# Optimization experiments

Hardware: AMD Instinct MI355X
Metric: run time of the kernel (lower is better)

Reference implementation:

```python
import jax, jax.numpy as jnp
import numpy as np

B = 2048   # number of samples; acts as seq_len for the (S,N,E) transformer
DIN = 768
D = 512    # hidden_dim
H = 8      # nheads
HD = D // H
L = 3      # encoder layers
P = 40     # num_prototypes
Q = D // 4 # 128, projected feature dim
EPS = 1e-5


def setup_inputs() -> dict:
    key = jax.random.key(0)
    ks = jax.random.split(key, 22)
    s = 0.02
    rn = lambda k, shape: jax.random.normal(k, shape, jnp.float32) * s
    return {
        "x": jax.random.normal(ks[0], (B, DIN), jnp.float32),
        "reduce_w": rn(ks[1], (D, DIN)), "reduce_b": rn(ks[2], (D,)),
        "in_w": rn(ks[3], (L, 3 * D, D)), "in_b": rn(ks[4], (L, 3 * D)),
        "out_w": rn(ks[5], (L, D, D)), "out_b": rn(ks[6], (L, D)),
        "ff1_w": rn(ks[7], (L, D, D)), "ff1_b": rn(ks[8], (L, D)),
        "ff2_w": rn(ks[9], (L, D, D)), "ff2_b": rn(ks[10], (L, D)),
        "ln1_w": jnp.ones((L, D), jnp.float32), "ln1_b": jnp.zeros((L, D), jnp.float32),
        "ln2_w": jnp.ones((L, D), jnp.float32), "ln2_b": jnp.zeros((L, D), jnp.float32),
        "mlp_w1": rn(ks[11], (D, D)), "mlp_b1": rn(ks[12], (D,)),
        "mlp_w2": rn(ks[13], (D, D)), "mlp_b2": rn(ks[14], (D,)),
        "mlp_w3": rn(ks[15], (Q, D)), "mlp_b3": rn(ks[16], (Q,)),
        "highlights": jax.random.normal(ks[17], (P, Q), jnp.float32),
        "negatives": jax.random.normal(ks[18], (P, Q), jnp.float32),
    }


def _inorm(x):
    # InstanceNorm1d (affine=False) on a 2D tensor: per-row normalize over last dim
    m = x.mean(-1, keepdims=True)
    v = ((x - m) ** 2).mean(-1, keepdims=True)  # biased variance, matches torch
    return (x - m) * jax.lax.rsqrt(v + EPS)


def _ln(x, w, b):
    m = x.mean(-1, keepdims=True)
    v = ((x - m) ** 2).mean(-1, keepdims=True)
    return (x - m) * jax.lax.rsqrt(v + EPS) * w + b


def _cdist(a, cb):
    # euclidean distances [B,P]
    d2 = (a * a).sum(-1, keepdims=True) + (cb * cb).sum(-1) - 2.0 * a @ cb.T
    return jnp.sqrt(jnp.maximum(d2, 0.0))


def reference(x, reduce_w, reduce_b, in_w, in_b, out_w, out_b,
              ff1_w, ff1_b, ff2_w, ff2_b, ln1_w, ln1_b, ln2_w, ln2_b,
              mlp_w1, mlp_b1, mlp_w2, mlp_b2, mlp_w3, mlp_b3,
              highlights, negatives):
    feat0 = _inorm(x @ reduce_w.T + reduce_b)  # [B,D]

    # TransformerEncoder, post-norm, relu FFN, dropout off (eval).
    # Input is (seq=B, batch=1, D) -> attention across all B rows.
    feat = feat0
    scale = 1.0 / np.sqrt(HD)
    for i in range(L):
        qkv = feat @ in_w[i].T + in_b[i]           # [B,3D]
        q, k, v = jnp.split(qkv, 3, axis=-1)
        q = q.reshape(B, H, HD)
        k = k.reshape(B, H, HD)
        v = v.reshape(B, H, HD)
        scores = jnp.einsum('ihd,jhd->hij', q, k) * scale  # [H,B,B]
        attn = jax.nn.softmax(scores, axis=-1)
        ctx = jnp.einsum('hij,jhd->ihd', attn, v).reshape(B, D)
        attn_out = ctx @ out_w[i].T + out_b[i]
        feat = _ln(feat + attn_out, ln1_w[i], ln1_b[i])
        ff = jax.nn.relu(feat @ ff1_w[i].T + ff1_b[i]) @ ff2_w[i].T + ff2_b[i]
        feat = _ln(feat + ff, ln2_w[i], ln2_b[i])

    feat = feat0 + _inorm(feat)

    # MLP 512 -> 512 -> 512 -> 128 (relu on all but last)
    feat = jax.nn.relu(feat @ mlp_w1.T + mlp_b1)
    feat = jax.nn.relu(feat @ mlp_w2.T + mlp_b2)
    feat = feat @ mlp_w3.T + mlp_b3
    feat = _inorm(feat)  # [B,Q]

    positive_dist = _cdist(feat, highlights).min(-1)
    negative_dist = _cdist(feat, negatives).min(-1)
    logits = jnp.stack([-negative_dist, -positive_dist], axis=-1)  # [B,2]
    return logits
```

## Files before the change

### kernel.cpp

```cpp
#include <hip/hip_runtime.h>
#include <math.h>
#include <cstddef>

#define EPS 1e-5f

typedef __attribute__((ext_vector_type(8))) short bf16x8;
typedef __attribute__((ext_vector_type(4))) float f32x4;

__device__ __forceinline__ float wave_sum(float v) {
#pragma unroll
  for (int o = 32; o > 0; o >>= 1) v += __shfl_xor(v, o, 64);
  return v;
}

__device__ __forceinline__ unsigned short f2b(float f) {
  union { float f; unsigned int u; } v; v.f = f;
  unsigned int r = (v.u + 0x7FFFu + ((v.u >> 16) & 1u)) >> 16;
  return (unsigned short)r;
}
__device__ __forceinline__ float b2f(unsigned short u) {
  union { unsigned int u; float f; } v; v.u = ((unsigned int)u) << 16;
  return v.f;
}

struct WConvArgs {
  const float* src[8];
  unsigned short* dst[8];
  int n[8];
};
__global__ __launch_bounds__(256) void conv_w(WConvArgs a) {
  const int arr = blockIdx.y;
  const int i = (blockIdx.x * 256 + threadIdx.x) * 4;
  if (i >= a.n[arr]) return;
  const float4 f = *(const float4*)(a.src[arr] + i);
  unsigned short t[4] = {f2b(f.x), f2b(f.y), f2b(f.z), f2b(f.w)};
  unsigned short* d = a.dst[arr] + i;
  *(ushort2*)d = *(ushort2*)&t[0];
  *(ushort2*)(d + 2) = *(ushort2*)&t[2];
}

template <int RELU, int AF32, int OUT_F32, int OUT_BF16, int MERGE, int RESID,
          int SCALEQ>
__global__ __launch_bounds__(256) void gemm32(
    const void* __restrict__ Aptr, const float* __restrict__ pmp,
    const unsigned short* __restrict__ W, const float* __restrict__ bias,
    const float* __restrict__ Rf, float* __restrict__ Cf,
    unsigned short* __restrict__ Cb, int M, int N, int K) {
  __shared__ __align__(16) unsigned short As[2][32][72];
  __shared__ __align__(16) unsigned short Ws[2][64][72];
  const int tid = threadIdx.x;
  const int wid = tid >> 6, lane = tid & 63;
  const int ln = lane & 15, quad = lane >> 4;
  const int m0 = blockIdx.x * 32, n0 = blockIdx.y * 64;
  const int arow = tid >> 3, aseg = tid & 7;
  const int wrow = tid >> 2, wseg = tid & 3;
  const int KS = K >> 6;

  bf16x8 ra;
  float4 ra32[2];
  bf16x8 rwb0, rwb1;
  bf16x8 rp[4];
  float rl;

  auto load_tile = [&](int ks) {
    const int k0 = ks * 64;
    if (MERGE) {
      const int h = ks;
      const int row = m0 + arow;
      rl = 0.f;
#pragma unroll
      for (int s = 0; s < 4; ++s) {
        const size_t b = (size_t)((s * 8 + h) * 2048 + row);
        rl += pmp[b];
        rp[s] = *(const bf16x8*)((const unsigned short*)Aptr + b * 64 + aseg * 8);
      }
    } else if (AF32) {
      const float* ap = (const float*)Aptr + (size_t)(m0 + arow) * K + k0 + aseg * 8;
      ra32[0] = *(const float4*)ap;
      ra32[1] = *(const float4*)(ap + 4);
    } else {
      ra = *(const bf16x8*)((const unsigned short*)Aptr +
                            (size_t)(m0 + arow) * K + k0 + aseg * 8);
    }
    const unsigned short* wp = W + (size_t)(n0 + wrow) * K + k0 + wseg * 16;
    rwb0 = *(const bf16x8*)wp;
    rwb1 = *(const bf16x8*)(wp + 8);
  };

  auto store_tile = [&](int buf) {
    if (MERGE) {
      float inv = 1.f / rl;
      unsigned short ta[8];
#pragma unroll
      for (int j = 0; j < 8; ++j) {
        float s = b2f((unsigned short)rp[0][j]) + b2f((unsigned short)rp[1][j]) +
                  b2f((unsigned short)rp[2][j]) + b2f((unsigned short)rp[3][j]);
        ta[j] = f2b(inv * s);
      }
      *(bf16x8*)&As[buf][arow][aseg * 8] = *(const bf16x8*)&ta[0];
    } else if (AF32) {
      unsigned short ta[8];
      ta[0] = f2b(ra32[0].x); ta[1] = f2b(ra32[0].y);
      ta[2] = f2b(ra32[0].z); ta[3] = f2b(ra32[0].w);
      ta[4] = f2b(ra32[1].x); ta[5] = f2b(ra32[1].y);
      ta[6] = f2b(ra32[1].z); ta[7] = f2b(ra32[1].w);
      *(bf16x8*)&As[buf][arow][aseg * 8] = *(const bf16x8*)&ta[0];
    } else {
      *(bf16x8*)&As[buf][arow][aseg * 8] = ra;
    }
    *(bf16x8*)&Ws[buf][wrow][wseg * 16] = rwb0;
    *(bf16x8*)&Ws[buf][wrow][wseg * 16 + 8] = rwb1;
  };

  f32x4 acc[2];
  acc[0] = (f32x4){0.f, 0.f, 0.f, 0.f};
  acc[1] = (f32x4){0.f, 0.f, 0.f, 0.f};

  const int mrow = (wid & 1) * 16, nh = wid >> 1;

  load_tile(0);
  store_tile(0);
  __syncthreads();

#pragma unroll 1
  for (int ks = 0; ks < KS; ++ks) {
    const int cur = ks & 1;
    if (ks + 1 < KS) load_tile(ks + 1);
#pragma unroll
    for (int kc = 0; kc < 2; ++kc) {
      bf16x8 af = *(const bf16x8*)&As[cur][mrow + ln][kc * 32 + quad * 8];
#pragma unroll
      for (int nt = 0; nt < 2; ++nt) {
        bf16x8 wf = *(const bf16x8*)&Ws[cur][nh * 32 + nt * 16 + ln][kc * 32 + quad * 8];
        acc[nt] = __builtin_amdgcn_mfma_f32_16x16x32_bf16(af, wf, acc[nt], 0, 0, 0);
      }
    }
    if (ks + 1 < KS) store_tile(cur ^ 1);
    __syncthreads();
  }

  const int gm = m0 + mrow + quad * 4;
  const float qs = (SCALEQ && n0 < 512) ? 0.125f : 1.f;
#pragma unroll
  for (int nt = 0; nt < 2; ++nt) {
    const int gn = n0 + nh * 32 + nt * 16 + ln;
    float bv = bias[gn];
#pragma unroll
    for (int r = 0; r < 4; ++r) {
      float v = acc[nt][r] + bv;
      if (SCALEQ) v *= qs;
      if (RELU) v = fmaxf(v, 0.f);
      if (RESID) v += Rf[(size_t)(gm + r) * N + gn];
      if (OUT_F32) Cf[(size_t)(gm + r) * N + gn] = v;
      if (OUT_BF16) Cb[(size_t)(gm + r) * N + gn] = f2b(v);
    }
  }
}

__global__ __launch_bounds__(256) void flash_attn7(
    const unsigned short* __restrict__ qkv, float* __restrict__ pm,
    unsigned short* __restrict__ po) {
  __shared__ __align__(16) unsigned short Ks[64][72];
  __shared__ __align__(16) unsigned short Vt[64][72];
  __shared__ __align__(16) unsigned short Ps[64][72];
  const int qt = blockIdx.x, h = blockIdx.y, sp = blockIdx.z;
  const int tid = threadIdx.x;
  const int wid = tid >> 6, lane = tid & 63;
  const int ln = lane & 15, quad = lane >> 4;
  const int wq0 = wid * 16;

  bf16x8 aq[2];
  {
    const unsigned short* qp =
        qkv + (size_t)(qt * 64 + wq0 + ln) * 1536 + h * 64 + quad * 8;
    aq[0] = *(const bf16x8*)qp;
    aq[1] = *(const bf16x8*)(qp + 32);
  }

  const int key = tid >> 2, seg = tid & 3;
  bf16x8 rk0, rk1;
  unsigned short tv[16];

  auto load_kv = [&](int t) {
    const int g = sp * 8 + t;
    const unsigned short* kr =
        qkv + (size_t)(g * 64 + key) * 1536 + 512 + h * 64 + seg * 16;
    rk0 = *(const bf16x8*)kr;
    rk1 = *(const bf16x8*)(kr + 8);
#pragma unroll
    for (int j = 0; j < 16; ++j)
      tv[j] = qkv[(size_t)(g * 64 + wid * 16 + j) * 1536 + 1024 + h * 64 + lane];
  };
  auto store_kv = [&]() {
    *(bf16x8*)&Ks[key][seg * 16] = rk0;
    *(bf16x8*)&Ks[key][seg * 16 + 8] = rk1;
    *(bf16x8*)&Vt[lane][wid * 16] = *(const bf16x8*)&tv[0];
    *(bf16x8*)&Vt[lane][wid * 16 + 8] = *(const bf16x8*)&tv[8];
  };

  float l_r[4] = {0.f, 0.f, 0.f, 0.f};
  f32x4 acc_o[4];
#pragma unroll
  for (int nt = 0; nt < 4; ++nt) acc_o[nt] = (f32x4){0.f, 0.f, 0.f, 0.f};

  load_kv(0);
  store_kv();
  __syncthreads();

#pragma unroll 1
  for (int t = 0; t < 8; ++t) {
    if (t + 1 < 8) load_kv(t + 1);

    f32x4 s_acc[4];
#pragma unroll
    for (int nt = 0; nt < 4; ++nt) s_acc[nt] = (f32x4){0.f, 0.f, 0.f, 0.f};
#pragma unroll
    for (int nt = 0; nt < 4; ++nt) {
      bf16x8 kf0 = *(const bf16x8*)&Ks[nt * 16 + ln][quad * 8];
      bf16x8 kf1 = *(const bf16x8*)&Ks[nt * 16 + ln][32 + quad * 8];
      s_acc[nt] = __builtin_amdgcn_mfma_f32_16x16x32_bf16(aq[0], kf0, s_acc[nt], 0, 0, 0);
      s_acc[nt] = __builtin_amdgcn_mfma_f32_16x16x32_bf16(aq[1], kf1, s_acc[nt], 0, 0, 0);
    }

#pragma unroll
    for (int nt = 0; nt < 4; ++nt) {
#pragma unroll
      for (int r = 0; r < 4; ++r) {
        float p = __expf(s_acc[nt][r]);
        l_r[r] += p;
        Ps[wq0 + quad * 4 + r][nt * 16 + ln] = f2b(p);
      }
    }

#pragma unroll
    for (int kc = 0; kc < 2; ++kc) {
      bf16x8 pf = *(const bf16x8*)&Ps[wq0 + ln][kc * 32 + quad * 8];
#pragma unroll
      for (int nt = 0; nt < 4; ++nt) {
        bf16x8 vf = *(const bf16x8*)&Vt[nt * 16 + ln][kc * 32 + quad * 8];
        acc_o[nt] = __builtin_amdgcn_mfma_f32_16x16x32_bf16(pf, vf, acc_o[nt], 0, 0, 0);
      }
    }
    __syncthreads();
    if (t + 1 < 8) {
      store_kv();
      __syncthreads();
    }
  }

  const size_t base = (size_t)((sp * 8 + h) * 2048 + qt * 64);
#pragma unroll
  for (int r = 0; r < 4; ++r) {
    float l = l_r[r];
    l += __shfl_xor(l, 1, 64);
    l += __shfl_xor(l, 2, 64);
    l += __shfl_xor(l, 4, 64);
    l += __shfl_xor(l, 8, 64);
    const size_t row = base + wq0 + quad * 4 + r;
    if (ln == 0) pm[row] = l;
#pragma unroll
    for (int nt = 0; nt < 4; ++nt)
      po[row * 64 + nt * 16 + ln] = f2b(acc_o[nt][r]);
  }
}

__global__ __launch_bounds__(256) void inorm512(float* __restrict__ dst,
                                                unsigned short* __restrict__ dstb,
                                                const float* __restrict__ src) {
  const int row = blockIdx.x * 4 + (threadIdx.x >> 6);
  const int lane = threadIdx.x & 63;
  const float4* s = (const float4*)(src + (size_t)row * 512);
  float4 a = s[lane], b = s[lane + 64];
  float sum = a.x + a.y + a.z + a.w + b.x + b.y + b.z + b.w;
  float mean = wave_sum(sum) * (1.f / 512.f);
  float vs = (a.x - mean) * (a.x - mean) + (a.y - mean) * (a.y - mean) +
             (a.z - mean) * (a.z - mean) + (a.w - mean) * (a.w - mean) +
             (b.x - mean) * (b.x - mean) + (b.y - mean) * (b.y - mean) +
             (b.z - mean) * (b.z - mean) + (b.w - mean) * (b.w - mean);
  float rs = rsqrtf(wave_sum(vs) * (1.f / 512.f) + EPS);
  float4 oa, obv;
  oa.x = (a.x - mean) * rs; oa.y = (a.y - mean) * rs;
  oa.z = (a.z - mean) * rs; oa.w = (a.w - mean) * rs;
  obv.x = (b.x - mean) * rs; obv.y = (b.y - mean) * rs;
  obv.z = (b.z - mean) * rs; obv.w = (b.w - mean) * rs;
  float4* d = (float4*)(dst + (size_t)row * 512);
  d[lane] = oa; d[lane + 64] = obv;
  unsigned short* db = dstb + (size_t)row * 512;
  unsigned short t0[4] = {f2b(oa.x), f2b(oa.y), f2b(oa.z), f2b(oa.w)};
  unsigned short t1[4] = {f2b(obv.x), f2b(obv.y), f2b(obv.z), f2b(obv.w)};
  *(ushort2*)&db[lane * 4] = *(ushort2*)&t0[0];
  *(ushort2*)&db[lane * 4 + 2] = *(ushort2*)&t0[2];
  *(ushort2*)&db[256 + lane * 4] = *(ushort2*)&t1[0];
  *(ushort2*)&db[256 + lane * 4 + 2] = *(ushort2*)&t1[2];
}

__global__ __launch_bounds__(256) void ln_res2(float* __restrict__ dst,
                                               unsigned short* __restrict__ dstb,
                                               const float* __restrict__ src,
                                               const float* __restrict__ w,
                                               const float* __restrict__ bb) {
  const int row = blockIdx.x * 4 + (threadIdx.x >> 6);
  const int lane = threadIdx.x & 63;
  const float4* xs = (const float4*)(src + (size_t)row * 512);
  float4 a = xs[lane], b = xs[lane + 64];
  float sum = a.x + a.y + a.z + a.w + b.x + b.y + b.z + b.w;
  float mean = wave_sum(sum) * (1.f / 512.f);
  float vs = (a.x - mean) * (a.x - mean) + (a.y - mean) * (a.y - mean) +
             (a.z - mean) * (a.z - mean) + (a.w - mean) * (a.w - mean) +
             (b.x - mean) * (b.x - mean) + (b.y - mean) * (b.y - mean) +
             (b.z - mean) * (b.z - mean) + (b.w - mean) * (b.w - mean);
  float rs = rsqrtf(wave_sum(vs) * (1.f / 512.f) + EPS);
  float4 wa = ((const float4*)w)[lane], wb = ((const float4*)w)[lane + 64];
  float4 ba = ((const float4*)bb)[lane], bbv = ((const float4*)bb)[lane + 64];
  float4 oa, ob2;
  oa.x = (a.x - mean) * rs * wa.x + ba.x; oa.y = (a.y - mean) * rs * wa.y + ba.y;
  oa.z = (a.z - mean) * rs * wa.z + ba.z; oa.w = (a.w - mean) * rs * wa.w + ba.w;
  ob2.x = (b.x - mean) * rs * wb.x + bbv.x; ob2.y = (b.y - mean) * rs * wb.y + bbv.y;
  ob2.z = (b.z - mean) * rs * wb.z + bbv.z; ob2.w = (b.w - mean) * rs * wb.w + bbv.w;
  float4* d = (float4*)(dst + (size_t)row * 512);
  d[lane] = oa; d[lane + 64] = ob2;
  unsigned short* dbp = dstb + (size_t)row * 512;
  unsigned short t0[4] = {f2b(oa.x), f2b(oa.y), f2b(oa.z), f2b(oa.w)};
  unsigned short t1[4] = {f2b(ob2.x), f2b(ob2.y), f2b(ob2.z), f2b(ob2.w)};
  *(ushort2*)&dbp[lane * 4] = *(ushort2*)&t0[0];
  *(ushort2*)&dbp[lane * 4 + 2] = *(ushort2*)&t0[2];
  *(ushort2*)&dbp[256 + lane * 4] = *(ushort2*)&t1[0];
  *(ushort2*)&dbp[256 + lane * 4 + 2] = *(ushort2*)&t1[2];
}

__global__ __launch_bounds__(256) void add_inorm(float* __restrict__ feat,
                                                 unsigned short* __restrict__ featb,
                                                 const float* __restrict__ feat0) {
  const int row = blockIdx.x * 4 + (threadIdx.x >> 6);
  const int lane = threadIdx.x & 63;
  float4* f = (float4*)(feat + (size_t)row * 512);
  const float4* f0 = (const float4*)(feat0 + (size_t)row * 512);
  float4 a = f[lane], b = f[lane + 64];
  float sum = a.x + a.y + a.z + a.w + b.x + b.y + b.z + b.w;
  float mean = wave_sum(sum) * (1.f / 512.f);
  float vs = (a.x - mean) * (a.x - mean) + (a.y - mean) * (a.y - mean) +
             (a.z - mean) * (a.z - mean) + (a.w - mean) * (a.w - mean) +
             (b.x - mean) * (b.x - mean) + (b.y - mean) * (b.y - mean) +
             (b.z - mean) * (b.z - mean) + (b.w - mean) * (b.w - mean);
  float rs = rsqrtf(wave_sum(vs) * (1.f / 512.f) + EPS);
  float4 za = f0[lane], zb = f0[lane + 64];
  float4 oa, ob2;
  oa.x = za.x + (a.x - mean) * rs; oa.y = za.y + (a.y - mean) * rs;
  oa.z = za.z + (a.z - mean) * rs; oa.w = za.w + (a.w - mean) * rs;
  ob2.x = zb.x + (b.x - mean) * rs; ob2.y = zb.y + (b.y - mean) * rs;
  ob2.z = zb.z + (b.z - mean) * rs; ob2.w = zb.w + (b.w - mean) * rs;
  f[lane] = oa; f[lane + 64] = ob2;
  unsigned short* dbp = featb + (size_t)row * 512;
  unsigned short t0[4] = {f2b(oa.x), f2b(oa.y), f2b(oa.z), f2b(oa.w)};
  unsigned short t1[4] = {f2b(ob2.x), f2b(ob2.y), f2b(ob2.z), f2b(ob2.w)};
  *(ushort2*)&dbp[lane * 4] = *(ushort2*)&t0[0];
  *(ushort2*)&dbp[lane * 4 + 2] = *(ushort2*)&t0[2];
  *(ushort2*)&dbp[256 + lane * 4] = *(ushort2*)&t1[0];
  *(ushort2*)&dbp[256 + lane * 4 + 2] = *(ushort2*)&t1[2];
}

__global__ __launch_bounds__(256) void dist2(const float* __restrict__ fq,
                                             const float* __restrict__ hi,
                                             const float* __restrict__ ne,
                                             float* __restrict__ out) {
  const int row = blockIdx.x * 4 + (threadIdx.x >> 6);
  const int lane = threadIdx.x & 63;
  float f0 = fq[(size_t)row * 128 + lane];
  float f1 = fq[(size_t)row * 128 + 64 + lane];
  float mean = wave_sum(f0 + f1) * (1.f / 128.f);
  float vs = (f0 - mean) * (f0 - mean) + (f1 - mean) * (f1 - mean);
  float rs = rsqrtf(wave_sum(vs) * (1.f / 128.f) + EPS);
  f0 = (f0 - mean) * rs;
  f1 = (f1 - mean) * rs;
  float mp = 1e30f, mn = 1e30f;
  for (int p = 0; p < 40; ++p) {
    float h0 = hi[p * 128 + lane], h1 = hi[p * 128 + 64 + lane];
    float d0 = f0 - h0, d1 = f1 - h1;
    float d2 = wave_sum(d0 * d0 + d1 * d1);
    mp = fminf(mp, d2);
    float n0 = ne[p * 128 + lane], n1 = ne[p * 128 + 64 + lane];
    d0 = f0 - n0; d1 = f1 - n1;
    d2 = wave_sum(d0 * d0 + d1 * d1);
    mn = fminf(mn, d2);
  }
  if (lane == 0) {
    out[row * 2 + 0] = -sqrtf(mn);
    out[row * 2 + 1] = -sqrtf(mp);
  }
}

extern "C" void kernel_launch(void* const* d_in, const int* in_sizes, int n_in,
                              void* d_out, int out_size, void* d_ws, size_t ws_size,
                              hipStream_t stream) {
  const float* x        = (const float*)d_in[0];
  const float* reduce_w = (const float*)d_in[1];
  const float* reduce_b = (const float*)d_in[2];
  const float* in_w     = (const float*)d_in[3];
  const float* in_b     = (const float*)d_in[4];
  const float* out_w    = (const float*)d_in[5];
  const float* out_b    = (const float*)d_in[6];
  const float* ff1_w    = (const float*)d_in[7];
  const float* ff1_b    = (const float*)d_in[8];
  const float* ff2_w    = (const float*)d_in[9];
  const float* ff2_b    = (const float*)d_in[10];
  const float* ln1_w    = (const float*)d_in[11];
  const float* ln1_b    = (const float*)d_in[12];
  const float* ln2_w    = (const float*)d_in[13];
  const float* ln2_b    = (const float*)d_in[14];
  const float* mlp_w1   = (const float*)d_in[15];
  const float* mlp_b1   = (const float*)d_in[16];
  const float* mlp_w2   = (const float*)d_in[17];
  const float* mlp_b2   = (const float*)d_in[18];
  const float* mlp_w3   = (const float*)d_in[19];
  const float* mlp_b3   = (const float*)d_in[20];
  const float* hi       = (const float*)d_in[21];
  const float* ne       = (const float*)d_in[22];
  float* out = (float*)d_out;
  float* ws = (float*)d_ws;

  const size_t MD = (size_t)2048 * 512;
  float* feat0_f = ws;
  float* feat_f  = ws + MD;
  float* tmp_f   = ws + 2 * MD;
  float* pm      = ws + 3 * MD;
  unsigned short* u = (unsigned short*)(ws + 3 * MD + 65536);
  unsigned short* qkv_b   = u;
  unsigned short* feat0_b = u + 3 * MD;
  unsigned short* feat_b  = u + 4 * MD;
  unsigned short* relu_b  = u + 5 * MD;
  unsigned short* po_b    = u + 6 * MD;
  unsigned short* relu2_b = qkv_b;
  float* featq_f = tmp_f;

  unsigned short* wb = u + 10 * MD;
  unsigned short* reduce_wb = wb;
  unsigned short* in_wb     = wb + 393216;
  unsigned short* out_wb    = in_wb + 2359296;
  unsigned short* ff1_wb    = out_wb + 786432;
  unsigned short* ff2_wb    = ff1_wb + 786432;
  unsigned short* mlp_w1b   = ff2_wb + 786432;
  unsigned short* mlp_w2b   = mlp_w1b + 262144;
  unsigned short* mlp_w3b   = mlp_w2b + 262144;

  dim3 blk(256);
  WConvArgs wa;
  wa.src[0] = reduce_w; wa.dst[0] = reduce_wb; wa.n[0] = 393216;
  wa.src[1] = in_w;     wa.dst[1] = in_wb;     wa.n[1] = 2359296;
  wa.src[2] = out_w;    wa.dst[2] = out_wb;    wa.n[2] = 786432;
  wa.src[3] = ff1_w;    wa.dst[3] = ff1_wb;    wa.n[3] = 786432;
  wa.src[4] = ff2_w;    wa.dst[4] = ff2_wb;    wa.n[4] = 786432;
  wa.src[5] = mlp_w1;   wa.dst[5] = mlp_w1b;   wa.n[5] = 262144;
  wa.src[6] = mlp_w2;   wa.dst[6] = mlp_w2b;   wa.n[6] = 262144;
  wa.src[7] = mlp_w3;   wa.dst[7] = mlp_w3b;   wa.n[7] = 65536;
  conv_w<<<dim3(2304, 8), blk, 0, stream>>>(wa);

  gemm32<0, 1, 1, 0, 0, 0, 0><<<dim3(64, 8), blk, 0, stream>>>(
      x, nullptr, reduce_wb, reduce_b, nullptr, feat0_f, nullptr, 2048, 512, 768);
  inorm512<<<512, blk, 0, stream>>>(feat0_f, feat0_b, feat0_f);

  for (int i = 0; i < 3; ++i) {
    const float* fin_f = (i == 0) ? feat0_f : feat_f;
    const unsigned short* fin_b = (i == 0) ? feat0_b : feat_b;
    gemm32<0, 0, 0, 1, 0, 0, 1><<<dim3(64, 24), blk, 0, stream>>>(
        fin_b, nullptr, in_wb + (size_t)i * 1536 * 512, in_b + i * 1536,
        nullptr, nullptr, qkv_b, 2048, 1536, 512);
    flash_attn7<<<dim3(32, 8, 4), blk, 0, stream>>>(qkv_b, pm, po_b);
    gemm32<0, 0, 1, 0, 1, 1, 0><<<dim3(64, 8), blk, 0, stream>>>(
        po_b, pm, out_wb + (size_t)i * 512 * 512, out_b + i * 512,
        fin_f, tmp_f, nullptr, 2048, 512, 512);
    ln_res2<<<512, blk, 0, stream>>>(feat_f, feat_b, tmp_f,
                                     ln1_w + i * 512, ln1_b + i * 512);
    gemm32<1, 0, 0, 1, 0, 0, 0><<<dim3(64, 8), blk, 0, stream>>>(
        feat_b, nullptr, ff1_wb + (size_t)i * 512 * 512, ff1_b + i * 512,
        nullptr, nullptr, relu_b, 2048, 512, 512);
    gemm32<0, 0, 1, 0, 0, 1, 0><<<dim3(64, 8), blk, 0, stream>>>(
        relu_b, nullptr, ff2_wb + (size_t)i * 512 * 512, ff2_b + i * 512,
        feat_f, tmp_f, nullptr, 2048, 512, 512);
    ln_res2<<<512, blk, 0, stream>>>(feat_f, feat_b, tmp_f,
                                     ln2_w + i * 512, ln2_b + i * 512);
  }

  add_inorm<<<512, blk, 0, stream>>>(feat_f, feat_b, feat0_f);
  gemm32<1, 0, 0, 1, 0, 0, 0><<<dim3(64, 8), blk, 0, stream>>>(
      feat_b, nullptr, mlp_w1b, mlp_b1, nullptr, nullptr, relu_b, 2048, 512, 512);
  gemm32<1, 0, 0, 1, 0, 0, 0><<<dim3(64, 8), blk, 0, stream>>>(
      relu_b, nullptr, mlp_w2b, mlp_b2, nullptr, nullptr, relu2_b, 2048, 512, 512);
  gemm32<0, 0, 1, 0, 0, 0, 0><<<dim3(64, 2), blk, 0, stream>>>(
      relu2_b, nullptr, mlp_w3b, mlp_b3, nullptr, featq_f, nullptr, 2048, 128, 512);
  dist2<<<512, blk, 0, stream>>>(featq_f, hi, ne, out);
}
```

Before: 365.0 us.

## Fuse layer/instance norms into GEMM epilogues and prologues via atomic row stats

Removes the standalone inorm and ln_res2 kernels. Each producing GEMM accumulates per-row sum and sum-of-squares with atomics, and the next GEMM applies the normalization while loading its A tile in fp32, writing the normalized fp32 copy once from the n0==0 blocks for later residual use. The final LN2 plus instance norm plus feat0 add is merged into one tail kernel. This saves launches and full-tensor passes, at the cost of atomics, fp32 A loads in GEMMs, and a less stable E[x^2]-mean^2 variance.

Result: slower. 383.7 us (+5.1%).

```diff
diff --git a/kernel.cpp b/kernel.cpp
--- a/kernel.cpp
+++ b/kernel.cpp
@@ -39,13 +39,20 @@
   *(ushort2*)(d + 2) = *(ushort2*)&t[2];
 }
 
-template <int RELU, int AF32, int OUT_F32, int OUT_BF16, int MERGE, int RESID,
-          int SCALEQ>
+__global__ __launch_bounds__(256) void zero_stats(float* __restrict__ st) {
+  st[blockIdx.x * 256 + threadIdx.x] = 0.f;
+}
+
+template <int RELU, int ASRC, int OUT_F32, int OUT_BF16, int RESID, int SCALEQ,
+          int STATS, int WF>
 __global__ __launch_bounds__(256) void gemm32(
     const void* __restrict__ Aptr, const float* __restrict__ pmp,
-    const unsigned short* __restrict__ W, const float* __restrict__ bias,
-    const float* __restrict__ Rf, float* __restrict__ Cf,
-    unsigned short* __restrict__ Cb, int M, int N, int K) {
+    const float* __restrict__ stA, const float* __restrict__ lnw,
+    const float* __restrict__ lnb, const unsigned short* __restrict__ W,
+    const float* __restrict__ bias, const float* __restrict__ Rf,
+    float* __restrict__ Cf, unsigned short* __restrict__ Cb,
+    float* __restrict__ stOut, float* __restrict__ finW,
+    int M, int N, int K) {
   __shared__ __align__(16) unsigned short As[2][32][72];
   __shared__ __align__(16) unsigned short Ws[2][64][72];
   const int tid = threadIdx.x;
@@ -58,13 +65,17 @@
 
   bf16x8 ra;
   float4 ra32[2];
+  float4 rlw[2], rlb[2];
+  float rmean, rrs;
   bf16x8 rwb0, rwb1;
   bf16x8 rp[4];
   float rl;
+  int curk0 = 0;
 
   auto load_tile = [&](int ks) {
     const int k0 = ks * 64;
-    if (MERGE) {
+    curk0 = k0;
+    if (ASRC == 2) {
       const int h = ks;
       const int row = m0 + arow;
       rl = 0.f;
@@ -74,10 +85,22 @@
         rl += pmp[b];
         rp[s] = *(const bf16x8*)((const unsigned short*)Aptr + b * 64 + aseg * 8);
       }
-    } else if (AF32) {
-      const float* ap = (const float*)Aptr + (size_t)(m0 + arow) * K + k0 + aseg * 8;
+    } else if (ASRC == 1 || ASRC == 3 || ASRC == 4) {
+      const int row = m0 + arow;
+      const float* ap = (const float*)Aptr + (size_t)row * K + k0 + aseg * 8;
       ra32[0] = *(const float4*)ap;
       ra32[1] = *(const float4*)(ap + 4);
+      if (ASRC == 3 || ASRC == 4) {
+        float s = stA[row * 2], q = stA[row * 2 + 1];
+        rmean = s * (1.f / 512.f);
+        rrs = rsqrtf(q * (1.f / 512.f) - rmean * rmean + EPS);
+        if (ASRC == 3) {
+          rlw[0] = *(const float4*)(lnw + k0 + aseg * 8);
+          rlw[1] = *(const float4*)(lnw + k0 + aseg * 8 + 4);
+          rlb[0] = *(const float4*)(lnb + k0 + aseg * 8);
+          rlb[1] = *(const float4*)(lnb + k0 + aseg * 8 + 4);
+        }
+      }
     } else {
       ra = *(const bf16x8*)((const unsigned short*)Aptr +
                             (size_t)(m0 + arow) * K + k0 + aseg * 8);
@@ -88,7 +111,7 @@
   };
 
   auto store_tile = [&](int buf) {
-    if (MERGE) {
+    if (ASRC == 2) {
       float inv = 1.f / rl;
       unsigned short ta[8];
 #pragma unroll
@@ -98,13 +121,36 @@
         ta[j] = f2b(inv * s);
       }
       *(bf16x8*)&As[buf][arow][aseg * 8] = *(const bf16x8*)&ta[0];
-    } else if (AF32) {
+    } else if (ASRC == 1 || ASRC == 3 || ASRC == 4) {
+      float zv[8] = {ra32[0].x, ra32[0].y, ra32[0].z, ra32[0].w,
+                     ra32[1].x, ra32[1].y, ra32[1].z, ra32[1].w};
+      float lwv[8], lbv[8];
+      if (ASRC == 3) {
+        lwv[0] = rlw[0].x; lwv[1] = rlw[0].y; lwv[2] = rlw[0].z; lwv[3] = rlw[0].w;
+        lwv[4] = rlw[1].x; lwv[5] = rlw[1].y; lwv[6] = rlw[1].z; lwv[7] = rlw[1].w;
+        lbv[0] = rlb[0].x; lbv[1] = rlb[0].y; lbv[2] = rlb[0].z; lbv[3] = rlb[0].w;
+        lbv[4] = rlb[1].x; lbv[5] = rlb[1].y; lbv[6] = rlb[1].z; lbv[7] = rlb[1].w;
+      }
+      float tv[8];
       unsigned short ta[8];
-      ta[0] = f2b(ra32[0].x); ta[1] = f2b(ra32[0].y);
-      ta[2] = f2b(ra32[0].z); ta[3] = f2b(ra32[0].w);
-      ta[4] = f2b(ra32[1].x); ta[5] = f2b(ra32[1].y);
-      ta[6] = f2b(ra32[1].z); ta[7] = f2b(ra32[1].w);
+#pragma unroll
+      for (int j = 0; j < 8; ++j) {
+        float t = zv[j];
+        if (ASRC == 3) t = (t - rmean) * rrs * lwv[j] + lbv[j];
+        if (ASRC == 4) t = (t - rmean) * rrs;
+        tv[j] = t;
+        ta[j] = f2b(t);
+      }
       *(bf16x8*)&As[buf][arow][aseg * 8] = *(const bf16x8*)&ta[0];
+      if (WF) {
+        if (n0 == 0) {
+          float* fp = finW + (size_t)(m0 + arow) * K + curk0 + aseg * 8;
+          float4 o0 = {tv[0], tv[1], tv[2], tv[3]};
+          float4 o1 = {tv[4], tv[5], tv[6], tv[7]};
+          *(float4*)fp = o0;
+          *(float4*)(fp + 4) = o1;
+        }
+      }
     } else {
       *(bf16x8*)&As[buf][arow][aseg * 8] = ra;
     }
@@ -141,6 +187,7 @@
 
   const int gm = m0 + mrow + quad * 4;
   const float qs = (SCALEQ && n0 < 512) ? 0.125f : 1.f;
+  float vbuf[2][4];
 #pragma unroll
   for (int nt = 0; nt < 2; ++nt) {
     const int gn = n0 + nh * 32 + nt * 16 + ln;
@@ -151,8 +198,24 @@
       if (SCALEQ) v *= qs;
       if (RELU) v = fmaxf(v, 0.f);
       if (RESID) v += Rf[(size_t)(gm + r) * N + gn];
+      vbuf[nt][r] = v;
       if (OUT_F32) Cf[(size_t)(gm + r) * N + gn] = v;
       if (OUT_BF16) Cb[(size_t)(gm + r) * N + gn] = f2b(v);
+    }
+  }
+  if (STATS) {
+#pragma unroll
+    for (int r = 0; r < 4; ++r) {
+      float s = vbuf[0][r] + vbuf[1][r];
+      float q = vbuf[0][r] * vbuf[0][r] + vbuf[1][r] * vbuf[1][r];
+      s += __shfl_xor(s, 1, 64); q += __shfl_xor(q, 1, 64);
+      s += __shfl_xor(s, 2, 64); q += __shfl_xor(q, 2, 64);
+      s += __shfl_xor(s, 4, 64); q += __shfl_xor(q, 4, 64);
+      s += __shfl_xor(s, 8, 64); q += __shfl_xor(q, 8, 64);
+      if (ln == 0) {
+        atomicAdd(&stOut[(gm + r) * 2], s);
+        atomicAdd(&stOut[(gm + r) * 2 + 1], q);
+      }
     }
   }
 }
@@ -264,95 +327,39 @@
   }
 }
 
-__global__ __launch_bounds__(256) void inorm512(float* __restrict__ dst,
-                                                unsigned short* __restrict__ dstb,
-                                                const float* __restrict__ src) {
+__global__ __launch_bounds__(256) void tail_fuse(
+    const float* __restrict__ z, const float* __restrict__ st,
+    const float* __restrict__ lnw, const float* __restrict__ lnb,
+    const float* __restrict__ feat0, unsigned short* __restrict__ outb) {
   const int row = blockIdx.x * 4 + (threadIdx.x >> 6);
   const int lane = threadIdx.x & 63;
-  const float4* s = (const float4*)(src + (size_t)row * 512);
-  float4 a = s[lane], b = s[lane + 64];
-  float sum = a.x + a.y + a.z + a.w + b.x + b.y + b.z + b.w;
+  const float4* zs = (const float4*)(z + (size_t)row * 512);
+  float4 a = zs[lane], b = zs[lane + 64];
+  const float mu = st[row * 2] * (1.f / 512.f);
+  const float rs = rsqrtf(st[row * 2 + 1] * (1.f / 512.f) - mu * mu + EPS);
+  float4 wa = ((const float4*)lnw)[lane], wb = ((const float4*)lnw)[lane + 64];
+  float4 ba = ((const float4*)lnb)[lane], bb = ((const float4*)lnb)[lane + 64];
+  float t[8];
+  t[0] = (a.x - mu) * rs * wa.x + ba.x; t[1] = (a.y - mu) * rs * wa.y + ba.y;
+  t[2] = (a.z - mu) * rs * wa.z + ba.z; t[3] = (a.w - mu) * rs * wa.w + ba.w;
+  t[4] = (b.x - mu) * rs * wb.x + bb.x; t[5] = (b.y - mu) * rs * wb.y + bb.y;
+  t[6] = (b.z - mu) * rs * wb.z + bb.z; t[7] = (b.w - mu) * rs * wb.w + bb.w;
+  float sum = t[0] + t[1] + t[2] + t[3] + t[4] + t[5] + t[6] + t[7];
   float mean = wave_sum(sum) * (1.f / 512.f);
-  float vs = (a.x - mean) * (a.x - mean) + (a.y - mean) * (a.y - mean) +
-             (a.z - mean) * (a.z - mean) + (a.w - mean) * (a.w - mean) +
-             (b.x - mean) * (b.x - mean) + (b.y - mean) * (b.y - mean) +
-             (b.z - mean) * (b.z - mean) + (b.w - mean) * (b.w - mean);
-  float rs = rsqrtf(wave_sum(vs) * (1.f / 512.f) + EPS);
-  float4 oa, obv;
-  oa.x = (a.x - mean) * rs; oa.y = (a.y - mean) * rs;
-  oa.z = (a.z - mean) * rs; oa.w = (a.w - mean) * rs;
-  obv.x = (b.x - mean) * rs; obv.y = (b.y - mean) * rs;
-  obv.z = (b.z - mean) * rs; obv.w = (b.w - mean) * rs;
-  float4* d = (float4*)(dst + (size_t)row * 512);
-  d[lane] = oa; d[lane + 64] = obv;
-  unsigned short* db = dstb + (size_t)row * 512;
-  unsigned short t0[4] = {f2b(oa.x), f2b(oa.y), f2b(oa.z), f2b(oa.w)};
-  unsigned short t1[4] = {f2b(obv.x), f2b(obv.y), f2b(obv.z), f2b(obv.w)};
-  *(ushort2*)&db[lane * 4] = *(ushort2*)&t0[0];
-  *(ushort2*)&db[lane * 4 + 2] = *(ushort2*)&t0[2];
-  *(ushort2*)&db[256 + lane * 4] = *(ushort2*)&t1[0];
-  *(ushort2*)&db[256 + lane * 4 + 2] = *(ushort2*)&t1[2];
-}
-
-__global__ __launch_bounds__(256) void ln_res2(float* __restrict__ dst,
-                                               unsigned short* __restrict__ dstb,
-                                               const float* __restrict__ src,
-                                               const float* __restrict__ w,
-                                               const float* __restrict__ bb) {
-  const int row = blockIdx.x * 4 + (threadIdx.x >> 6);
-  const int lane = threadIdx.x & 63;
-  const float4* xs = (const float4*)(src + (size_t)row * 512);
-  float4 a = xs[lane], b = xs[lane + 64];
-  float sum = a.x + a.y + a.z + a.w + b.x + b.y + b.z + b.w;
-  float mean = wave_sum(sum) * (1.f / 512.f);
-  float vs = (a.x - mean) * (a.x - mean) + (a.y - mean) * (a.y - mean) +
-             (a.z - mean) * (a.z - mean) + (a.w - mean) * (a.w - mean) +
-             (b.x - mean) * (b.x - mean) + (b.y - mean) * (b.y - mean) +
-             (b.z - mean) * (b.z - mean) + (b.w - mean) * (b.w - mean);
-  float rs = rsqrtf(wave_sum(vs) * (1.f / 512.f) + EPS);
-  float4 wa = ((const float4*)w)[lane], wb = ((const float4*)w)[lane + 64];
-  float4 ba = ((const float4*)bb)[lane], bbv = ((const float4*)bb)[lane + 64];
-  float4 oa, ob2;
-  oa.x = (a.x - mean) * rs * wa.x + ba.x; oa.y = (a.y - mean) * rs * wa.y + ba.y;
-  oa.z = (a.z - mean) * rs * wa.z + ba.z; oa.w = (a.w - mean) * rs * wa.w + ba.w;
-  ob2.x = (b.x - mean) * rs * wb.x + bbv.x; ob2.y = (b.y - mean) * rs * wb.y + bbv.y;
-  ob2.z = (b.z - mean) * rs * wb.z + bbv.z; ob2.w = (b.w - mean) * rs * wb.w + bbv.w;
-  float4* d = (float4*)(dst + (size_t)row * 512);
-  d[lane] = oa; d[lane + 64] = ob2;
-  unsigned short* dbp = dstb + (size_t)row * 512;
-  unsigned short t0[4] = {f2b(oa.x), f2b(oa.y), f2b(oa.z), f2b(oa.w)};
-  unsigned short t1[4] = {f2b(ob2.x), f2b(ob2.y), f2b(ob2.z), f2b(ob2.w)};
-  *(ushort2*)&dbp[lane * 4] = *(ushort2*)&t0[0];
-  *(ushort2*)&dbp[lane * 4 + 2] = *(ushort2*)&t0[2];
-  *(ushort2*)&dbp[256 + lane * 4] = *(ushort2*)&t1[0];
-  *(ushort2*)&dbp[256 + lane * 4 + 2] = *(ushort2*)&t1[2];
-}
-
-__global__ __launch_bounds__(256) void add_inorm(float* __restrict__ feat,
-                                                 unsigned short* __restrict__ featb,
-                                                 const float* __restrict__ feat0) {
-  const int row = blockIdx.x * 4 + (threadIdx.x >> 6);
-  const int lane = threadIdx.x & 63;
-  float4* f = (float4*)(feat + (size_t)row * 512);
+  float vs = 0.f;
+#pragma unroll
+  for (int j = 0; j < 8; ++j) vs += (t[j] - mean) * (t[j] - mean);
+  float rs2 = rsqrtf(wave_sum(vs) * (1.f / 512.f) + EPS);
   const float4* f0 = (const float4*)(feat0 + (size_t)row * 512);
-  float4 a = f[lane], b = f[lane + 64];
-  float sum = a.x + a.y + a.z + a.w + b.x + b.y + b.z + b.w;
-  float mean = wave_sum(sum) * (1.f / 512.f);
-  float vs = (a.x - mean) * (a.x - mean) + (a.y - mean) * (a.y - mean) +
-             (a.z - mean) * (a.z - mean) + (a.w - mean) * (a.w - mean) +
-             (b.x - mean) * (b.x - mean) + (b.y - mean) * (b.y - mean) +
-             (b.z - mean) * (b.z - mean) + (b.w - mean) * (b.w - mean);
-  float rs = rsqrtf(wave_sum(vs) * (1.f / 512.f) + EPS);
   float4 za = f0[lane], zb = f0[lane + 64];
-  float4 oa, ob2;
-  oa.x = za.x + (a.x - mean) * rs; oa.y = za.y + (a.y - mean) * rs;
-  oa.z = za.z + (a.z - mean) * rs; oa.w = za.w + (a.w - mean) * rs;
-  ob2.x = zb.x + (b.x - mean) * rs; ob2.y = zb.y + (b.y - mean) * rs;
-  ob2.z = zb.z + (b.z - mean) * rs; ob2.w = zb.w + (b.w - mean) * rs;
-  f[lane] = oa; f[lane + 64] = ob2;
-  unsigned short* dbp = featb + (size_t)row * 512;
-  unsigned short t0[4] = {f2b(oa.x), f2b(oa.y), f2b(oa.z), f2b(oa.w)};
-  unsigned short t1[4] = {f2b(ob2.x), f2b(ob2.y), f2b(ob2.z), f2b(ob2.w)};
+  float o[8];
+  o[0] = za.x + (t[0] - mean) * rs2; o[1] = za.y + (t[1] - mean) * rs2;
+  o[2] = za.z + (t[2] - mean) * rs2; o[3] = za.w + (t[3] - mean) * rs2;
+  o[4] = zb.x + (t[4] - mean) * rs2; o[5] = zb.y + (t[5] - mean) * rs2;
+  o[6] = zb.z + (t[6] - mean) * rs2; o[7] = zb.w + (t[7] - mean) * rs2;
+  unsigned short* dbp = outb + (size_t)row * 512;
+  unsigned short t0[4] = {f2b(o[0]), f2b(o[1]), f2b(o[2]), f2b(o[3])};
+  unsigned short t1[4] = {f2b(o[4]), f2b(o[5]), f2b(o[6]), f2b(o[7])};
   *(ushort2*)&dbp[lane * 4] = *(ushort2*)&t0[0];
   *(ushort2*)&dbp[lane * 4 + 2] = *(ushort2*)&t0[2];
   *(ushort2*)&dbp[256 + lane * 4] = *(ushort2*)&t1[0];
@@ -420,19 +427,22 @@
 
   const size_t MD = (size_t)2048 * 512;
   float* feat0_f = ws;
-  float* feat_f  = ws + MD;
-  float* tmp_f   = ws + 2 * MD;
-  float* pm      = ws + 3 * MD;
-  unsigned short* u = (unsigned short*)(ws + 3 * MD + 65536);
+  float* fin_f   = ws + MD;
+  float* feat_f  = ws + 2 * MD;
+  float* zr      = ws + 3 * MD;
+  float* zA      = ws + 4 * MD;
+  float* zB      = ws + 5 * MD;
+  float* pm      = ws + 6 * MD;
+  float* st      = ws + 6 * MD + 65536;
+  unsigned short* u = (unsigned short*)(ws + 6 * MD + 65536 + 7 * 4096);
   unsigned short* qkv_b   = u;
-  unsigned short* feat0_b = u + 3 * MD;
-  unsigned short* feat_b  = u + 4 * MD;
-  unsigned short* relu_b  = u + 5 * MD;
-  unsigned short* po_b    = u + 6 * MD;
+  unsigned short* relu_b  = u + 3 * MD;
+  unsigned short* mlpin_b = u + 4 * MD;
+  unsigned short* po_b    = u + 5 * MD;
   unsigned short* relu2_b = qkv_b;
-  float* featq_f = tmp_f;
-
-  unsigned short* wb = u + 10 * MD;
+  float* featq_f = zr;
+
+  unsigned short* wb = u + 9 * MD;
   unsigned short* reduce_wb = wb;
   unsigned short* in_wb     = wb + 393216;
   unsigned short* out_wb    = in_wb + 2359296;
@@ -441,6 +451,10 @@
   unsigned short* mlp_w1b   = ff2_wb + 786432;
   unsigned short* mlp_w2b   = mlp_w1b + 262144;
   unsigned short* mlp_w3b   = mlp_w2b + 262144;
+
+  float* st0  = st;
+  auto stA = [&](int i) { return st + 4096 * (1 + 2 * i); };
+  auto stB = [&](int i) { return st + 4096 * (2 + 2 * i); };
 
   dim3 blk(256);
   WConvArgs wa;
@@ -453,39 +467,48 @@
   wa.src[6] = mlp_w2;   wa.dst[6] = mlp_w2b;   wa.n[6] = 262144;
   wa.src[7] = mlp_w3;   wa.dst[7] = mlp_w3b;   wa.n[7] = 65536;
   conv_w<<<dim3(2304, 8), blk, 0, stream>>>(wa);
-
-  gemm32<0, 1, 1, 0, 0, 0, 0><<<dim3(64, 8), blk, 0, stream>>>(
-      x, nullptr, reduce_wb, reduce_b, nullptr, feat0_f, nullptr, 2048, 512, 768);
-  inorm512<<<512, blk, 0, stream>>>(feat0_f, feat0_b, feat0_f);
+  zero_stats<<<112, blk, 0, stream>>>(st);
+
+  gemm32<0, 1, 1, 0, 0, 0, 1, 0><<<dim3(64, 8), blk, 0, stream>>>(
+      x, nullptr, nullptr, nullptr, nullptr, reduce_wb, reduce_b, nullptr,
+      zr, nullptr, st0, nullptr, 2048, 512, 768);
 
   for (int i = 0; i < 3; ++i) {
-    const float* fin_f = (i == 0) ? feat0_f : feat_f;
-    const unsigned short* fin_b = (i == 0) ? feat0_b : feat_b;
-    gemm32<0, 0, 0, 1, 0, 0, 1><<<dim3(64, 24), blk, 0, stream>>>(
-        fin_b, nullptr, in_wb + (size_t)i * 1536 * 512, in_b + i * 1536,
-        nullptr, nullptr, qkv_b, 2048, 1536, 512);
+    if (i == 0) {
+      gemm32<0, 4, 0, 1, 0, 1, 0, 1><<<dim3(64, 24), blk, 0, stream>>>(
+          zr, nullptr, st0, nullptr, nullptr, in_wb, in_b,
+          nullptr, nullptr, qkv_b, nullptr, feat0_f, 2048, 1536, 512);
+    } else {
+      gemm32<0, 3, 0, 1, 0, 1, 0, 1><<<dim3(64, 24), blk, 0, stream>>>(
+          zB, nullptr, stB(i - 1), ln2_w + (i - 1) * 512, ln2_b + (i - 1) * 512,
+          in_wb + (size_t)i * 1536 * 512, in_b + i * 1536,
+          nullptr, nullptr, qkv_b, nullptr, fin_f, 2048, 1536, 512);
+    }
     flash_attn7<<<dim3(32, 8, 4), blk, 0, stream>>>(qkv_b, pm, po_b);
-    gemm32<0, 0, 1, 0, 1, 1, 0><<<dim3(64, 8), blk, 0, stream>>>(
-        po_b, pm, out_wb + (size_t)i * 512 * 512, out_b + i * 512,
-        fin_f, tmp_f, nullptr, 2048, 512, 512);
-    ln_res2<<<512, blk, 0, stream>>>(feat_f, feat_b, tmp_f,
-                                     ln1_w + i * 512, ln1_b + i * 512);
-    gemm32<1, 0, 0, 1, 0, 0, 0><<<dim3(64, 8), blk, 0, stream>>>(
-        feat_b, nullptr, ff1_wb + (size_t)i * 512 * 512, ff1_b + i * 512,
-        nullptr, nullptr, relu_b, 2048, 512, 512);
-    gemm32<0, 0, 1, 0, 0, 1, 0><<<dim3(64, 8), blk, 0, stream>>>(
-        relu_b, nullptr, ff2_wb + (size_t)i * 512 * 512, ff2_b + i * 512,
-        feat_f, tmp_f, nullptr, 2048, 512, 512);
-    ln_res2<<<512, blk, 0, stream>>>(feat_f, feat_b, tmp_f,
-                                     ln2_w + i * 512, ln2_b + i * 512);
-  }
-
-  add_inorm<<<512, blk, 0, stream>>>(feat_f, feat_b, feat0_f);
-  gemm32<1, 0, 0, 1, 0, 0, 0><<<dim3(64, 8), blk, 0, stream>>>(
-      feat_b, nullptr, mlp_w1b, mlp_b1, nullptr, nullptr, relu_b, 2048, 512, 512);
-  gemm32<1, 0, 0, 1, 0, 0, 0><<<dim3(64, 8), blk, 0, stream>>>(
-      relu_b, nullptr, mlp_w2b, mlp_b2, nullptr, nullptr, relu2_b, 2048, 512, 512);
-  gemm32<0, 0, 1, 0, 0, 0, 0><<<dim3(64, 2), blk, 0, stream>>>(
-      relu2_b, nullptr, mlp_w3b, mlp_b3, nullptr, featq_f, nullptr, 2048, 128, 512);
+    const float* resid1 = (i == 0) ? feat0_f : fin_f;
+    gemm32<0, 2, 1, 0, 1, 0, 1, 0><<<dim3(64, 8), blk, 0, stream>>>(
+        po_b, pm, nullptr, nullptr, nullptr, out_wb + (size_t)i * 512 * 512,
+        out_b + i * 512, resid1, zA, nullptr, stA(i), nullptr, 2048, 512, 512);
+    gemm32<1, 3, 0, 1, 0, 0, 0, 1><<<dim3(64, 8), blk, 0, stream>>>(
+        zA, nullptr, stA(i), ln1_w + i * 512, ln1_b + i * 512,
+        ff1_wb + (size_t)i * 512 * 512, ff1_b + i * 512,
+        nullptr, nullptr, relu_b, nullptr, feat_f, 2048, 512, 512);
+    gemm32<0, 0, 1, 0, 1, 0, 1, 0><<<dim3(64, 8), blk, 0, stream>>>(
+        relu_b, nullptr, nullptr, nullptr, nullptr,
+        ff2_wb + (size_t)i * 512 * 512, ff2_b + i * 512,
+        feat_f, zB, nullptr, stB(i), nullptr, 2048, 512, 512);
+  }
+
+  tail_fuse<<<512, blk, 0, stream>>>(zB, stB(2), ln2_w + 2 * 512,
+                                     ln2_b + 2 * 512, feat0_f, mlpin_b);
+  gemm32<1, 0, 0, 1, 0, 0, 0, 0><<<dim3(64, 8), blk, 0, stream>>>(
+      mlpin_b, nullptr, nullptr, nullptr, nullptr, mlp_w1b, mlp_b1,
+      nullptr, nullptr, relu_b, nullptr, nullptr, 2048, 512, 512);
+  gemm32<1, 0, 0, 1, 0, 0, 0, 0><<<dim3(64, 8), blk, 0, stream>>>(
+      relu_b, nullptr, nullptr, nullptr, nullptr, mlp_w2b, mlp_b2,
+      nullptr, nullptr, relu2_b, nullptr, nullptr, 2048, 512, 512);
+  gemm32<0, 0, 1, 0, 0, 0, 0, 0><<<dim3(64, 2), blk, 0, stream>>>(
+      relu2_b, nullptr, nullptr, nullptr, nullptr, mlp_w3b, mlp_b3,
+      nullptr, featq_f, nullptr, nullptr, nullptr, 2048, 128, 512);
   dist2<<<512, blk, 0, stream>>>(featq_f, hi, ne, out);
 }
```
